# Performance work log

Hardware: AMD Instinct MI355X
Metric: run time of the kernel (lower is better)

## Reference

```python
import jax, jax.numpy as jnp
import numpy as np

D_MODEL = 1024
MAX_NUM_LAYERS = 4


def setup_inputs() -> dict:
    key = jax.random.key(0)
    ks = jax.random.split(key, 8)
    S, B, D, L = 1024, 2, D_MODEL, 3
    w = lambda k: (jax.random.normal(k, (D, D), dtype=jnp.float32) * 0.02)
    return {
        "x": jax.random.normal(ks[0], (S, B, D), dtype=jnp.float32),
        "layer_outputs": jax.random.normal(ks[1], (L, S, B, D), dtype=jnp.float32),
        "Wq": w(ks[2]), "bq": jnp.zeros((D,), jnp.float32),
        "Wk": w(ks[3]), "bk": jnp.zeros((D,), jnp.float32),
        "Wv": w(ks[4]), "bv": jnp.zeros((D,), jnp.float32),
        "Wo": w(ks[5]), "bo": jnp.zeros((D,), jnp.float32),
        "layer_weights": jnp.ones((MAX_NUM_LAYERS + 1,), jnp.float32),
        "num_heads": 16,
    }


def reference(x, layer_outputs, Wq, bq, Wk, bk, Wv, bv, Wo, bo, layer_weights, num_heads):
    # x: [S, B, D]; layer_outputs: [L, S, B, D] (stacked prev layer outputs)
    S, B, D = x.shape
    H = num_heads
    hd = D // H
    scale = hd ** -0.5
    # q from x only: [S, B*H, hd] -> [BH, S, hd]
    q = (x @ Wq.T + bq).reshape(S, B * H, hd).transpose(1, 0, 2)
    # k/v from x and all previous layer outputs (shared K/V projections)
    xs = jnp.concatenate([x[None], layer_outputs], axis=0)          # [Lp1, S, B, D]
    Lp1 = xs.shape[0]
    k = (xs @ Wk.T + bk).reshape(Lp1, S, B * H, hd).transpose(0, 2, 1, 3)  # [Lp1, BH, S, hd]
    v = (xs @ Wv.T + bv).reshape(Lp1, S, B * H, hd).transpose(0, 2, 1, 3)
    # per-layer scores, softmax over the key axis (torch dim=-2 of stacked scores)
    scores = jnp.einsum('bqd,lbkd->lbqk', q, k) * scale             # [Lp1, BH, S, S]
    attn = jax.nn.softmax(scores, axis=-1)
    lw = jax.nn.softmax(layer_weights[:Lp1])                        # [Lp1]
    combined = jnp.einsum('l,lbqk,lbkd->bqd', lw, attn, v)          # [BH, S, hd]
    combined = combined.transpose(1, 0, 2).reshape(S, B, D)
    return combined @ Wo.T + bo
```

## Files before the change

kernel.cpp:

```cpp
#include <hip/hip_runtime.h>
#include <hip/hip_bf16.h>
#include <math.h>

#define S_LEN   1024
#define BATCH   2
#define DMODEL  1024
#define NHEADS  16
#define HDIM    64
#define BHEADS  32
#define LP1     4
#define ROWS_PL 2048

typedef __attribute__((ext_vector_type(8)))  short bf16x8;
typedef __attribute__((ext_vector_type(4)))  float f32x4;
typedef __attribute__((ext_vector_type(16))) float f32x16;

__device__ inline ushort bf16_rne(float a) {
    unsigned u = __float_as_uint(a);
    return (ushort)((u + 0x7FFFu + ((u >> 16) & 1u)) >> 16);
}
__device__ inline float bf16_up(ushort h) { return __uint_as_float(((unsigned)h) << 16); }
__device__ inline void split_bf16(float a, ushort &hi, ushort &lo) {
    hi = bf16_rne(a);
    lo = bf16_rne(a - bf16_up(hi));
}
__device__ inline uint pk_bf16(float a, float b) {
    float2 f; f.x = a; f.y = b;
    __hip_bfloat162 h = __float22bfloat162_rn(f);
    return *reinterpret_cast<uint*>(&h);
}
#if __has_builtin(__builtin_amdgcn_exp2f)
__device__ inline float fast_exp2(float x) { return __builtin_amdgcn_exp2f(x); }
#else
__device__ inline float fast_exp2(float x) { return exp2f(x); }
#endif

__device__ inline void permswap(uint &a, uint &b) {
    asm("v_permlane32_swap_b32 %0, %1" : "+v"(a), "+v"(b));
}

__device__ inline void glds16(const ushort* g, ushort* l) {
    __builtin_amdgcn_global_load_lds(
        (const __attribute__((address_space(1))) void*)g,
        (__attribute__((address_space(3))) void*)l, 16, 0, 0);
}

#define SCLF 0.18033688011112042f

__global__ __launch_bounds__(256)
void presplit(const float* __restrict__ x, const float* __restrict__ lo,
              const float* __restrict__ Wq, const float* __restrict__ Wk,
              const float* __restrict__ Wv, const float* __restrict__ Wo,
              ushort* __restrict__ XsH, ushort* __restrict__ WH,
              ushort* __restrict__ WL)
{
    const int z = blockIdx.z;
    const float* src; ushort* dh; ushort* dl = nullptr; int n;
    if (z == 0)      { src = x;  dh = XsH;           n = 2097152; }
    else if (z == 1) { src = lo; dh = XsH + 2097152; n = 6291456; }
    else {
        const float* wsrc[4] = { Wq, Wk, Wv, Wo };
        src = wsrc[z - 2];
        dh = WH + (size_t)(z - 2) * 1048576;
        if (z == 2 || z == 5) dl = WL + (size_t)(z - 2) * 1048576;
        n = 1048576;
    }
    const int i = (blockIdx.x * 256 + threadIdx.x) * 8;
    if (i >= n) return;
    float v[8];
    *(float4*)&v[0] = *(const float4*)(src + i);
    *(float4*)&v[4] = *(const float4*)(src + i + 4);
    ushort h[8];
    #pragma unroll
    for (int j = 0; j < 8; ++j) h[j] = bf16_rne(v[j]);
    *(uint4*)(dh + i) = *(uint4*)h;
    if (dl) {
        ushort l[8];
        #pragma unroll
        for (int j = 0; j < 8; ++j) l[j] = bf16_rne(v[j] - bf16_up(h[j]));
        *(uint4*)(dl + i) = *(uint4*)l;
    }
}

__global__ __launch_bounds__(256, 2)
void proj_qkv(const ushort* __restrict__ XsH,
              const ushort* __restrict__ WH, const ushort* __restrict__ WL,
              const float* __restrict__ bq, const float* __restrict__ bk,
              const float* __restrict__ bv,
              ushort* __restrict__ qhb, ushort* __restrict__ qlb,
              ushort* __restrict__ kout, ushort* __restrict__ vout)
{
    __shared__ ushort smem[2][12288];
    const int bid = blockIdx.x;
    const int t   = threadIdx.x;
    const int wv  = t >> 6, lane = t & 63;
    const int quad = lane >> 4, r = lane & 15;
    const int lrow = lane >> 2;
    const int lch  = ((lane & 3) ^ (lrow & 3) ^ ((lrow >> 2) & 3)) * 8;
    const int q0x  = ((quad ^ (r & 3) ^ ((r >> 2) & 3)) << 3);
    const int cn   = lane & 15;

    if (bid >= 512) {
        const int fid = bid - 512;
        const int nt = (fid & 7) * 2 + ((fid >> 3) & 1);
        const int mt = fid >> 4;
        const int m0 = mt * 64, n0 = nt * 64;

        const int wm = wv & 1, wn = wv >> 1;
        const int mBase = wm * 32, nBase = wn * 32;

        const ushort* Asrc  = XsH + (size_t)(m0 + wv * 16 + lrow) * DMODEL + lch;
        const ushort* Bhsrc = WH  + (size_t)(n0 + wv * 16 + lrow) * DMODEL + lch;
        const ushort* Blsrc = WL  + (size_t)(n0 + wv * 16 + lrow) * DMODEL + lch;

        f32x4 acc[2][2];
        #pragma unroll
        for (int i = 0; i < 2; ++i)
            #pragma unroll
            for (int j = 0; j < 2; ++j) acc[i][j] = (f32x4){0.f, 0.f, 0.f, 0.f};

        glds16(Asrc,  smem[0]        + wv * 512);
        glds16(Bhsrc, smem[0] + 2048 + wv * 512);
        glds16(Blsrc, smem[0] + 4096 + wv * 512);

        for (int k = 0; k < 32; ++k) {
            const int cur = k & 1;
            __syncthreads();
            if (k + 1 < 32) {
                const int off = (k + 1) * 32;
                glds16(Asrc  + off, smem[cur ^ 1]        + wv * 512);
                glds16(Bhsrc + off, smem[cur ^ 1] + 2048 + wv * 512);
                glds16(Blsrc + off, smem[cur ^ 1] + 4096 + wv * 512);
            }
            const ushort* Ah = smem[cur];
            const ushort* Bh = smem[cur] + 2048;
            const ushort* Bl = smem[cur] + 4096;
            bf16x8 fa[2], fbh[2], fbl[2];
            #pragma unroll
            for (int i = 0; i < 2; ++i)
                fa[i] = *(const bf16x8*)&Ah[(mBase + i * 16 + r) * 32 + q0x];
            #pragma unroll
            for (int j = 0; j < 2; ++j) {
                fbh[j] = *(const bf16x8*)&Bh[(nBase + j * 16 + r) * 32 + q0x];
                fbl[j] = *(const bf16x8*)&Bl[(nBase + j * 16 + r) * 32 + q0x];
            }
            #pragma unroll
            for (int i = 0; i < 2; ++i)
                #pragma unroll
                for (int j = 0; j < 2; ++j) {
                    acc[i][j] = __builtin_amdgcn_mfma_f32_16x16x32_bf16(fa[i], fbh[j], acc[i][j], 0, 0, 0);
                    acc[i][j] = __builtin_amdgcn_mfma_f32_16x16x32_bf16(fa[i], fbl[j], acc[i][j], 0, 0, 0);
                }
        }

        #pragma unroll
        for (int j = 0; j < 2; ++j) {
            const int n = n0 + nBase + j * 16 + cn;
            const float bvv = bq[n];
            #pragma unroll
            for (int i = 0; i < 2; ++i) {
                const int mrow = m0 + mBase + i * 16 + quad * 4;
                #pragma unroll
                for (int g = 0; g < 4; ++g) {
                    const int m = mrow + g;
                    const float val = (acc[i][j][g] + bvv) * SCLF;
                    const int s = m >> 1, b = m & 1;
                    const int bh = b * 16 + (n >> 6), e = n & 63;
                    const size_t idx = (((size_t)bh * S_LEN) + s) * HDIM + e;
                    ushort hi, lov; split_bf16(val, hi, lov);
                    qhb[idx] = hi; qlb[idx] = lov;
                }
            }
        }
    } else {
        const int fid = bid;
        const int n0 = (fid & 7) * 128;
        const int m0 = (fid >> 3) * 128;
        const int lyr = m0 >> 11;

        const int wm = wv & 1, wn = wv >> 1;
        const int mBase = wm * 64, nBase = wn * 64;

        const ushort* KWh = WH + 1048576;
        const ushort* VWh = WH + 2097152;
        const ushort* Asrc0 = XsH + (size_t)(m0 + wv * 16 + lrow) * DMODEL + lch;
        const ushort* Asrc1 = Asrc0 + (size_t)64 * DMODEL;
        const ushort* Bw[2] = { KWh, VWh };
        const ushort* Bsrc[2][2];
        #pragma unroll
        for (int p = 0; p < 2; ++p)
            #pragma unroll
            for (int seg = 0; seg < 2; ++seg)
                Bsrc[p][seg] = Bw[p] + (size_t)(n0 + wv * 32 + seg * 16 + lrow) * DMODEL + lch;

        f32x4 aK[4][4], aV[4][4];
        #pragma unroll
        for (int i = 0; i < 4; ++i)
            #pragma unroll
            for (int j = 0; j < 4; ++j) {
                aK[i][j] = (f32x4){0.f, 0.f, 0.f, 0.f};
                aV[i][j] = (f32x4){0.f, 0.f, 0.f, 0.f};
            }

        glds16(Asrc0, smem[0]        + wv * 512);
        glds16(Asrc1, smem[0] + 2048 + wv * 512);
        #pragma unroll
        for (int p = 0; p < 2; ++p)
            #pragma unroll
            for (int seg = 0; seg < 2; ++seg)
                glds16(Bsrc[p][seg], smem[0] + 4096 + p * 4096 + (wv * 2 + seg) * 512);

        for (int k = 0; k < 32; ++k) {
            const int cur = k & 1;
            __syncthreads();
            if (k + 1 < 32) {
                const int off = (k + 1) * 32;
                glds16(Asrc0 + off, smem[cur ^ 1]        + wv * 512);
                glds16(Asrc1 + off, smem[cur ^ 1] + 2048 + wv * 512);
                #pragma unroll
                for (int p = 0; p < 2; ++p)
                    #pragma unroll
                    for (int seg = 0; seg < 2; ++seg)
                        glds16(Bsrc[p][seg] + off,
                               smem[cur ^ 1] + 4096 + p * 4096 + (wv * 2 + seg) * 512);
            }
            const ushort* Ah = smem[cur];
            const ushort* Bp = smem[cur] + 4096;

            bf16x8 fa[4];
            #pragma unroll
            for (int i = 0; i < 4; ++i)
                fa[i] = *(const bf16x8*)&Ah[(mBase + i * 16 + r) * 32 + q0x];
            #pragma unroll
            for (int j = 0; j < 4; ++j) {
                const int off2 = (nBase + j * 16 + r) * 32 + q0x;
                const bf16x8 fkh = *(const bf16x8*)&Bp[off2];
                const bf16x8 fvh = *(const bf16x8*)&Bp[4096 + off2];
                #pragma unroll
                for (int i = 0; i < 4; ++i) {
                    aK[i][j] = __builtin_amdgcn_mfma_f32_16x16x32_bf16(fa[i], fkh, aK[i][j], 0, 0, 0);
                    aV[i][j] = __builtin_amdgcn_mfma_f32_16x16x32_bf16(fa[i], fvh, aV[i][j], 0, 0, 0);
                }
            }
        }

        #pragma unroll
        for (int j = 0; j < 4; ++j) {
            const int n = n0 + nBase + j * 16 + cn;
            const float bb = bk[n];
            const int e    = n & 63;
            const int es_k = e >> 4, half_k = (e >> 3) & 1, j_k = e & 7;
            const int h    = n >> 6;
            #pragma unroll
            for (int i = 0; i < 4; ++i) {
                #pragma unroll
                for (int g = 0; g < 4; ++g) {
                    const int m = m0 + mBase + i * 16 + quad * 4 + g;
                    const int rem = m & 2047, s = rem >> 1, b = rem & 1;
                    const int bhI = lyr * 32 + b * 16 + h;
                    const int kt  = s >> 5;
                    const int lnk = half_k * 32 + (s & 31);
                    kout[(size_t)bhI * 65536 + (size_t)(kt * 4 + es_k) * 512 + lnk * 8 + j_k]
                        = bf16_rne(aK[i][j][g] + bb);
                }
            }
        }

        ushort* T = &smem[0][0];
        __syncthreads();
        #pragma unroll
        for (int j = 0; j < 4; ++j) {
            const int nloc = nBase + j * 16 + cn;
            const float bb = bv[n0 + nloc];
            #pragma unroll
            for (int i = 0; i < 4; ++i) {
                #pragma unroll
                for (int g = 0; g < 4; ++g) {
                    const int mloc = mBase + i * 16 + quad * 4 + g;
                    T[nloc * 130 + mloc] = bf16_rne(aV[i][j][g] + bb);
                }
            }
        }
        __syncthreads();
        {
            const int nloc = t >> 1, bsel = t & 1;
            const int n = n0 + nloc, h = n >> 6;
            const int e = n & 63;
            const int dg = e >> 5, lid_v = e & 31;
            const int s0g = (m0 & 2047) >> 1;
            const int kt0 = s0g >> 5;
            const int bhI = lyr * 32 + bsel * 16 + h;
            #pragma unroll
            for (int c = 0; c < 8; ++c) {
                ushort tmp[8];
                #pragma unroll
                for (int j = 0; j < 8; ++j)
                    tmp[j] = T[nloc * 130 + 2 * (c * 8 + j) + bsel];
                const int kt = kt0 + (c >> 2);
                const int c2 = c & 3;
                const int ks = c2 >> 1, hv = c2 & 1;
                ushort* dstb = vout + (size_t)bhI * 65536 + (size_t)kt * 2048;
                *(uint4*)(dstb + (ks * 2 + dg) * 512 + (hv * 32 + lid_v) * 8) = *(uint4*)tmp;
            }
        }
    }
}

__global__ __launch_bounds__(256)
void proj_o(const ushort* __restrict__ Abf,
            const ushort* __restrict__ Bhg, const ushort* __restrict__ Blg,
            const float* __restrict__ bias, float* __restrict__ outf)
{
    __shared__ ushort smem[2][3 * 2048];

    const int fid = blockIdx.x;
    const int nt = (fid & 7) * 2 + ((fid >> 3) & 1);
    const int mt = fid >> 4;
    const int m0 = mt * 64, n0 = nt * 64;

    const int t  = threadIdx.x;
    const int wv = t >> 6, lane = t & 63;
    const int quad = lane >> 4, r = lane & 15;
    const int wm = wv & 1, wn = wv >> 1;
    const int mBase = wm * 32, nBase = wn * 32;

    const int lrow = lane >> 2;
    const int lch  = ((lane & 3) ^ (lrow & 3) ^ ((lrow >> 2) & 3)) * 8;
    const ushort* Asrc  = Abf + (size_t)(m0 + wv * 16 + lrow) * DMODEL + lch;
    const ushort* Bhsrc = Bhg + (size_t)(n0 + wv * 16 + lrow) * DMODEL + lch;
    const ushort* Blsrc = Blg + (size_t)(n0 + wv * 16 + lrow) * DMODEL + lch;

    const int q0x = ((quad ^ (r & 3) ^ ((r >> 2) & 3)) << 3);
    f32x4 acc[2][2];
    #pragma unroll
    for (int i = 0; i < 2; ++i)
        #pragma unroll
        for (int j = 0; j < 2; ++j) acc[i][j] = (f32x4){0.f, 0.f, 0.f, 0.f};

    glds16(Asrc,  smem[0]        + wv * 512);
    glds16(Bhsrc, smem[0] + 2048 + wv * 512);
    glds16(Blsrc, smem[0] + 4096 + wv * 512);

    for (int k = 0; k < 32; ++k) {
        const int cur = k & 1;
        __syncthreads();
        if (k + 1 < 32) {
            const int off = (k + 1) * 32;
            glds16(Asrc  + off, smem[cur ^ 1]        + wv * 512);
            glds16(Bhsrc + off, smem[cur ^ 1] + 2048 + wv * 512);
            glds16(Blsrc + off, smem[cur ^ 1] + 4096 + wv * 512);
        }
        const ushort* Ah = smem[cur];
        const ushort* Bh = smem[cur] + 2048;
        const ushort* Bl = smem[cur] + 4096;
        bf16x8 fa[2], fbh[2], fbl[2];
        #pragma unroll
        for (int i = 0; i < 2; ++i)
            fa[i] = *(const bf16x8*)&Ah[(mBase + i * 16 + r) * 32 + q0x];
        #pragma unroll
        for (int j = 0; j < 2; ++j) {
            fbh[j] = *(const bf16x8*)&Bh[(nBase + j * 16 + r) * 32 + q0x];
            fbl[j] = *(const bf16x8*)&Bl[(nBase + j * 16 + r) * 32 + q0x];
        }
        #pragma unroll
        for (int i = 0; i < 2; ++i)
            #pragma unroll
            for (int j = 0; j < 2; ++j) {
                acc[i][j] = __builtin_amdgcn_mfma_f32_16x16x32_bf16(fa[i], fbh[j], acc[i][j], 0, 0, 0);
                acc[i][j] = __builtin_amdgcn_mfma_f32_16x16x32_bf16(fa[i], fbl[j], acc[i][j], 0, 0, 0);
            }
    }

    const int cn = lane & 15;
    #pragma unroll
    for (int j = 0; j < 2; ++j) {
        const int n = n0 + nBase + j * 16 + cn;
        const float bvv = bias[n];
        #pragma unroll
        for (int i = 0; i < 2; ++i) {
            const int mrow = m0 + mBase + i * 16 + quad * 4;
            #pragma unroll
            for (int g = 0; g < 4; ++g)
                outf[(size_t)(mrow + g) * DMODEL + n] = acc[i][j][g] + bvv;
        }
    }
}

__global__ __launch_bounds__(256, 2)
void attn_mfma(const ushort* __restrict__ qhg, const ushort* __restrict__ qlg,
               const ushort* __restrict__ kh, const ushort* __restrict__ vth,
               const float* __restrict__ lwraw, float* __restrict__ part)
{
    const int t    = threadIdx.x;
    const int wv   = t >> 6, lane = t & 63;
    const int half = lane >> 5, lid = lane & 31;

    const int fid  = blockIdx.x;
    const int xcd  = fid & 7, slot = fid >> 3;
    const int pair = xcd * 16 + (slot >> 2);
    const int qt   = slot & 3;
    const int bh   = pair & 31, l = pair >> 5;
    const int qbase = qt * 256 + wv * 64;

    float wl;
    {
        float v[LP1], wm = -3.0e38f;
        #pragma unroll
        for (int i = 0; i < LP1; ++i) { v[i] = lwraw[i]; wm = fmaxf(wm, v[i]); }
        float ws = 0.f;
        #pragma unroll
        for (int i = 0; i < LP1; ++i) { v[i] = __expf(v[i] - wm); ws += v[i]; }
        wl = v[l] / ws;
    }

    bf16x8 qh[2][4], ql[2][4];
    #pragma unroll
    for (int u = 0; u < 2; ++u) {
        const size_t qoff = ((size_t)bh * S_LEN + qbase + u * 32 + lid) * HDIM + half * 8;
        #pragma unroll
        for (int es = 0; es < 4; ++es) {
            qh[u][es] = *(const bf16x8*)(qhg + qoff + es * 16);
            ql[u][es] = *(const bf16x8*)(qlg + qoff + es * 16);
        }
    }

    f32x16 o[2][2];
    #pragma unroll
    for (int u = 0; u < 2; ++u)
        #pragma unroll
        for (int dg = 0; dg < 2; ++dg)
            #pragma unroll
            for (int i = 0; i < 16; ++i) o[u][dg][i] = 0.f;
    float ls[2] = {0.f, 0.f};

    f32x16 zf;
    #pragma unroll
    for (int i = 0; i < 16; ++i) zf[i] = 0.f;

    const size_t kvo = (size_t)(l * BHEADS + bh) * S_LEN * HDIM;
    const ushort* kfb = kh  + kvo + (size_t)lane * 8;
    const ushort* vfb = vth + kvo + (size_t)lane * 8;

    bf16x8 kb[4], kn[4];
    #pragma unroll
    for (int es = 0; es < 4; ++es)
        kb[es] = *(const bf16x8*)(kfb + es * 512);
    #pragma unroll
    for (int es = 0; es < 4; ++es)
        kn[es] = *(const bf16x8*)(kfb + 2048 + es * 512);

    f32x16 sa[2];
    #pragma unroll
    for (int es = 0; es < 4; ++es)
        #pragma unroll
        for (int u = 0; u < 2; ++u) {
            sa[u] = __builtin_amdgcn_mfma_f32_32x32x16_bf16(kb[es], qh[u][es],
                                                            es == 0 ? zf : sa[u], 0, 0, 0);
            sa[u] = __builtin_amdgcn_mfma_f32_32x32x16_bf16(kb[es], ql[u][es], sa[u], 0, 0, 0);
        }

    for (int kt = 0; kt < 32; ++kt) {
        bf16x8 vb[2][2];
        {
            const ushort* vp = vfb + (size_t)kt * 2048;
            #pragma unroll
            for (int ks = 0; ks < 2; ++ks)
                #pragma unroll
                for (int dg = 0; dg < 2; ++dg)
                    vb[ks][dg] = *(const bf16x8*)(vp + (ks * 2 + dg) * 512);
        }

        bf16x8 pf[2][2];
        #pragma unroll
        for (int ks = 0; ks < 2; ++ks) {
            #pragma unroll
            for (int u = 0; u < 2; ++u) {
                const float p0 = fast_exp2(sa[u][8 * ks + 0]);
                const float p1 = fast_exp2(sa[u][8 * ks + 1]);
                const float p2 = fast_exp2(sa[u][8 * ks + 2]);
                const float p3 = fast_exp2(sa[u][8 * ks + 3]);
                const float p4 = fast_exp2(sa[u][8 * ks + 4]);
                const float p5 = fast_exp2(sa[u][8 * ks + 5]);
                const float p6 = fast_exp2(sa[u][8 * ks + 6]);
                const float p7 = fast_exp2(sa[u][8 * ks + 7]);
                ls[u] += ((p0 + p1) + (p2 + p3)) + ((p4 + p5) + (p6 + p7));

                uint a0 = pk_bf16(p0, p1);
                uint a1 = pk_bf16(p2, p3);
                uint b0 = pk_bf16(p4, p5);
                uint b1 = pk_bf16(p6, p7);
                permswap(a0, b0);
                permswap(a1, b1);
                union { uint w[4]; bf16x8 v; } pu;
                pu.w[0] = a0; pu.w[1] = a1; pu.w[2] = b0; pu.w[3] = b1;
                pf[ks][u] = pu.v;
            }
        }

        #pragma unroll
        for (int es = 0; es < 4; ++es) kb[es] = kn[es];
        {
            const ushort* kp = kfb + (size_t)((kt + 2) & 31) * 2048;
            #pragma unroll
            for (int es = 0; es < 4; ++es) kn[es] = *(const bf16x8*)(kp + es * 512);
        }

        __builtin_amdgcn_s_setprio(1);
        #pragma unroll
        for (int es = 0; es < 4; ++es)
            #pragma unroll
            for (int u = 0; u < 2; ++u) {
                sa[u] = __builtin_amdgcn_mfma_f32_32x32x16_bf16(kb[es], qh[u][es],
                                                                es == 0 ? zf : sa[u], 0, 0, 0);
                sa[u] = __builtin_amdgcn_mfma_f32_32x32x16_bf16(kb[es], ql[u][es], sa[u], 0, 0, 0);
            }
        __builtin_amdgcn_s_setprio(0);

        __builtin_amdgcn_s_setprio(1);
        #pragma unroll
        for (int ks = 0; ks < 2; ++ks)
            #pragma unroll
            for (int dg = 0; dg < 2; ++dg)
                #pragma unroll
                for (int u = 0; u < 2; ++u)
                    o[u][dg] = __builtin_amdgcn_mfma_f32_32x32x16_bf16(vb[ks][dg], pf[ks][u], o[u][dg], 0, 0, 0);
        __builtin_amdgcn_s_setprio(0);
    }

    const int b = bh >> 4, hh = bh & 15;
    #pragma unroll
    for (int u = 0; u < 2; ++u) {
        float lsv = ls[u];
        lsv += __shfl_xor(lsv, 32);
        const float sc = wl / lsv;
        const int q = qbase + u * 32 + lid;
        float* pb = part + (size_t)l * (ROWS_PL * DMODEL)
                  + ((size_t)q * BATCH + b) * DMODEL + hh * HDIM;
        #pragma unroll
        for (int dg = 0; dg < 2; ++dg)
            #pragma unroll
            for (int rq = 0; rq < 4; ++rq) {
                float4 vv;
                vv.x = o[u][dg][rq * 4 + 0] * sc;
                vv.y = o[u][dg][rq * 4 + 1] * sc;
                vv.z = o[u][dg][rq * 4 + 2] * sc;
                vv.w = o[u][dg][rq * 4 + 3] * sc;
                *(float4*)(pb + dg * 32 + rq * 8 + half * 4) = vv;
            }
    }
}

__global__ __launch_bounds__(256)
void sum_y(const float* __restrict__ part, ushort* __restrict__ YH)
{
    const int i = (blockIdx.x * 256 + threadIdx.x) * 8;
    float acc[8];
    #pragma unroll
    for (int c = 0; c < 2; ++c) {
        float4 s = *(const float4*)(part + i + c * 4);
        #pragma unroll
        for (int l = 1; l < LP1; ++l) {
            const float4 p = *(const float4*)(part + (size_t)l * 2097152 + i + c * 4);
            s.x += p.x; s.y += p.y; s.z += p.z; s.w += p.w;
        }
        acc[c * 4 + 0] = s.x; acc[c * 4 + 1] = s.y;
        acc[c * 4 + 2] = s.z; acc[c * 4 + 3] = s.w;
    }
    uint out[4];
    #pragma unroll
    for (int c = 0; c < 4; ++c) out[c] = pk_bf16(acc[c * 2], acc[c * 2 + 1]);
    *(uint4*)(YH + i) = *(uint4*)out;
}

extern "C" void kernel_launch(void* const* d_in, const int* in_sizes, int n_in,
                              void* d_out, int out_size, void* d_ws, size_t ws_size,
                              hipStream_t stream) {
    const float* x  = (const float*)d_in[0];
    const float* lo = (const float*)d_in[1];
    const float* Wq = (const float*)d_in[2];
    const float* bq = (const float*)d_in[3];
    const float* Wk = (const float*)d_in[4];
    const float* bk = (const float*)d_in[5];
    const float* Wv = (const float*)d_in[6];
    const float* bv = (const float*)d_in[7];
    const float* Wo = (const float*)d_in[8];
    const float* bo = (const float*)d_in[9];
    const float* lw = (const float*)d_in[10];
    float* out = (float*)d_out;

    char* ws = (char*)d_ws;
    ushort* XsH  = (ushort*)(ws);
    ushort* WH   = (ushort*)(ws + 16777216);
    ushort* WL   = (ushort*)(ws + 25165824);
    ushort* qhb  = (ushort*)(ws + 33554432);
    ushort* qlb  = (ushort*)(ws + 37748736);
    ushort* khb  = (ushort*)(ws + 41943040);
    ushort* vthb = (ushort*)(ws + 58720256);
    float*  part = (float*)(ws + 75497472);
    ushort* YH   = (ushort*)(ws + 109051904);

    dim3 blk(256);
    presplit<<<dim3(3072, 1, 6), blk, 0, stream>>>(x, lo, Wq, Wk, Wv, Wo, XsH, WH, WL);
    proj_qkv<<<dim3(1024), blk, 0, stream>>>(XsH, WH, WL, bq, bk, bv,
                                             qhb, qlb, khb, vthb);
    attn_mfma<<<dim3(512), blk, 0, stream>>>(qhb, qlb, khb, vthb, lw, part);
    sum_y<<<dim3(1024), blk, 0, stream>>>(part, YH);
    proj_o<<<dim3(512), blk, 0, stream>>>(YH, WH + 3145728, WL + 3145728, bo, out);
}
```

Measured before the change: 234.9 us.

## Split attention key range across wave pairs and combine partials in LDS

The attention kernel now splits the key dimension across two waves per query tile, so each wave walks 16 key tiles instead of 32. The grid doubles to 1024 blocks, with 128 queries per block instead of 256, and launch bounds ask for 4 blocks per CU. Partial outputs and row sums from the second wave group are added into the first through shared memory and two barriers, then written out. This is meant to raise parallelism and occupancy and shorten the serial loop, at the cost of extra LDS traffic, synchronization and register pressure from the tighter launch bound. Because the softmax has no max subtraction, partial sums can be added directly.

```diff
diff --git a/kernel.cpp b/kernel.cpp
--- a/kernel.cpp
+++ b/kernel.cpp
@@ -386,21 +386,25 @@
     }
 }
 
-__global__ __launch_bounds__(256, 2)
+__global__ __launch_bounds__(256, 4)
 void attn_mfma(const ushort* __restrict__ qhg, const ushort* __restrict__ qlg,
                const ushort* __restrict__ kh, const ushort* __restrict__ vth,
                const float* __restrict__ lwraw, float* __restrict__ part)
 {
+    __shared__ float cmb[2][33 * 64];
+
     const int t    = threadIdx.x;
     const int wv   = t >> 6, lane = t & 63;
     const int half = lane >> 5, lid = lane & 31;
+    const int wq   = wv & 1;
+    const int wk   = wv >> 1;
 
     const int fid  = blockIdx.x;
     const int xcd  = fid & 7, slot = fid >> 3;
-    const int pair = xcd * 16 + (slot >> 2);
-    const int qt   = slot & 3;
+    const int pair = xcd * 16 + (slot >> 3);
+    const int qt   = slot & 7;
     const int bh   = pair & 31, l = pair >> 5;
-    const int qbase = qt * 256 + wv * 64;
+    const int qbase = qt * 128 + wq * 64;
 
     float wl;
     {
@@ -440,14 +444,15 @@
     const size_t kvo = (size_t)(l * BHEADS + bh) * S_LEN * HDIM;
     const ushort* kfb = kh  + kvo + (size_t)lane * 8;
     const ushort* vfb = vth + kvo + (size_t)lane * 8;
+    const int kt0 = wk * 16;
 
     bf16x8 kb[4], kn[4];
     #pragma unroll
     for (int es = 0; es < 4; ++es)
-        kb[es] = *(const bf16x8*)(kfb + es * 512);
+        kb[es] = *(const bf16x8*)(kfb + (size_t)kt0 * 2048 + es * 512);
     #pragma unroll
     for (int es = 0; es < 4; ++es)
-        kn[es] = *(const bf16x8*)(kfb + 2048 + es * 512);
+        kn[es] = *(const bf16x8*)(kfb + (size_t)(kt0 + 1) * 2048 + es * 512);
 
     f32x16 sa[2];
     #pragma unroll
@@ -459,7 +464,8 @@
             sa[u] = __builtin_amdgcn_mfma_f32_32x32x16_bf16(kb[es], ql[u][es], sa[u], 0, 0, 0);
         }
 
-    for (int kt = 0; kt < 32; ++kt) {
+    for (int it = 0; it < 16; ++it) {
+        const int kt = kt0 + it;
         bf16x8 vb[2][2];
         {
             const ushort* vp = vfb + (size_t)kt * 2048;
@@ -500,7 +506,7 @@
         #pragma unroll
         for (int es = 0; es < 4; ++es) kb[es] = kn[es];
         {
-            const ushort* kp = kfb + (size_t)((kt + 2) & 31) * 2048;
+            const ushort* kp = kfb + (size_t)(kt0 + ((it + 2) & 15)) * 2048;
             #pragma unroll
             for (int es = 0; es < 4; ++es) kn[es] = *(const bf16x8*)(kp + es * 512);
         }
@@ -527,26 +533,58 @@
         __builtin_amdgcn_s_setprio(0);
     }
 
-    const int b = bh >> 4, hh = bh & 15;
+    float lsv[2];
     #pragma unroll
     for (int u = 0; u < 2; ++u) {
-        float lsv = ls[u];
-        lsv += __shfl_xor(lsv, 32);
-        const float sc = wl / lsv;
-        const int q = qbase + u * 32 + lid;
-        float* pb = part + (size_t)l * (ROWS_PL * DMODEL)
-                  + ((size_t)q * BATCH + b) * DMODEL + hh * HDIM;
-        #pragma unroll
-        for (int dg = 0; dg < 2; ++dg)
-            #pragma unroll
-            for (int rq = 0; rq < 4; ++rq) {
-                float4 vv;
-                vv.x = o[u][dg][rq * 4 + 0] * sc;
-                vv.y = o[u][dg][rq * 4 + 1] * sc;
-                vv.z = o[u][dg][rq * 4 + 2] * sc;
-                vv.w = o[u][dg][rq * 4 + 3] * sc;
-                *(float4*)(pb + dg * 32 + rq * 8 + half * 4) = vv;
-            }
+        float v = ls[u];
+        v += __shfl_xor(v, 32);
+        lsv[u] = v;
+    }
+
+    #pragma unroll
+    for (int u = 0; u < 2; ++u) {
+        if (wk == 1) {
+            float* dst = &cmb[wq][0];
+            #pragma unroll
+            for (int dg = 0; dg < 2; ++dg)
+                #pragma unroll
+                for (int i = 0; i < 16; ++i)
+                    dst[(dg * 16 + i) * 64 + lane] = o[u][dg][i];
+            dst[32 * 64 + lane] = lsv[u];
+        }
+        __syncthreads();
+        if (wk == 0) {
+            const float* src = &cmb[wq][0];
+            #pragma unroll
+            for (int dg = 0; dg < 2; ++dg)
+                #pragma unroll
+                for (int i = 0; i < 16; ++i)
+                    o[u][dg][i] += src[(dg * 16 + i) * 64 + lane];
+            lsv[u] += src[32 * 64 + lane];
+        }
+        __syncthreads();
+    }
+
+    if (wk == 0) {
+        const int b = bh >> 4, hh = bh & 15;
+        #pragma unroll
+        for (int u = 0; u < 2; ++u) {
+            const float sc = wl / lsv[u];
+            const int q = qbase + u * 32 + lid;
+            float* pb = part + (size_t)l * (ROWS_PL * DMODEL)
+                      + ((size_t)q * BATCH + b) * DMODEL + hh * HDIM;
+            #pragma unroll
+            for (int dg = 0; dg < 2; ++dg)
+                #pragma unroll
+                for (int rq = 0; rq < 4; ++rq) {
+                    float4 vv;
+                    vv.x = o[u][dg][rq * 4 + 0] * sc;
+                    vv.y = o[u][dg][rq * 4 + 1] * sc;
+                    vv.z = o[u][dg][rq * 4 + 2] * sc;
+                    vv.w = o[u][dg][rq * 4 + 3] * sc;
+                    *(float4*)(pb + dg * 32 + rq * 8 + half * 4) = vv;
+                }
+        }
     }
 }
 
@@ -603,7 +641,7 @@
     presplit<<<dim3(3072, 1, 6), blk, 0, stream>>>(x, lo, Wq, Wk, Wv, Wo, XsH, WH, WL);
     proj_qkv<<<dim3(1024), blk, 0, stream>>>(XsH, WH, WL, bq, bk, bv,
                                              qhb, qlb, khb, vthb);
-    attn_mfma<<<dim3(512), blk, 0, stream>>>(qhb, qlb, khb, vthb, lw, part);
+    attn_mfma<<<dim3(1024), blk, 0, stream>>>(qhb, qlb, khb, vthb, lw, part);
     sum_y<<<dim3(1024), blk, 0, stream>>>(part, YH);
     proj_o<<<dim3(512), blk, 0, stream>>>(YH, WH + 3145728, WL + 3145728, bo, out);
 }
```

Result: slower. 648.8 us (+176.3%).
